# Kernel optimization log

Measured on AMD Instinct MI355X. Metric: run time of the kernel, lower is better.

## Reference

```python
import jax, jax.numpy as jnp
import numpy as np

NTOKENS = 50257
NHID = 1024
NPC = int(np.ceil(np.sqrt(NTOKENS)))            # 225 tokens per class
NCLASSES = int(np.ceil(NTOKENS / NPC))          # 224 classes
BATCH = 1024
INITRANGE = 0.1


def setup_inputs() -> dict:
    key = jax.random.key(0)
    k1, k2, k3, k4 = jax.random.split(key, 4)
    inputs = jax.random.normal(k1, (BATCH, NHID), dtype=jnp.float32)
    labels = jax.random.randint(k2, (BATCH,), 0, NTOKENS, dtype=jnp.int64)
    layer_top_W = jax.random.uniform(k3, (NHID, NCLASSES), minval=-INITRANGE, maxval=INITRANGE, dtype=jnp.float32)
    layer_top_b = jnp.zeros((NCLASSES,), dtype=jnp.float32)
    layer_bottom_W = jax.random.uniform(k4, (NCLASSES, NHID, NPC), minval=-INITRANGE, maxval=INITRANGE, dtype=jnp.float32)
    layer_bottom_b = jnp.zeros((NCLASSES, NPC), dtype=jnp.float32)
    return {
        "inputs": inputs,
        "labels": labels,
        "layer_top_W": layer_top_W,
        "layer_top_b": layer_top_b,
        "layer_bottom_W": layer_bottom_W,
        "layer_bottom_b": layer_bottom_b,
    }


def reference(inputs, labels, layer_top_W, layer_top_b, layer_bottom_W, layer_bottom_b):
    batch_size = inputs.shape[0]
    # decompose label into (class, within-class) position; old-torch `/` on Long == floor div
    pos_top = labels // NPC            # [B]
    pos_bottom = labels % NPC          # [B]

    # top-level class distribution: [B, nclasses]
    top_logits = inputs @ layer_top_W + layer_top_b
    top_probs = jax.nn.softmax(top_logits, axis=1)

    # gather per-sample class weight slices and do batched matvec:
    # layer_bottom_W[pos_top]: [B, nhid, npc]
    bottom_logits = jnp.einsum("bd,bdc->bc", inputs, layer_bottom_W[pos_top]) + layer_bottom_b[pos_top]
    bottom_probs = jax.nn.softmax(bottom_logits, axis=1)

    rows = jnp.arange(batch_size)
    target_probs = top_probs[rows, pos_top] * bottom_probs[rows, pos_bottom]  # [B]
    return target_probs
```

## Files before the change

kernel.cpp:

```cpp
#include <hip/hip_runtime.h>
#include <math.h>

#define NHID 1024
#define NPC  225
#define NCLS 224
#define BATCH 1024
#define NBLK  256

typedef float f4u __attribute__((ext_vector_type(4), aligned(4)));

#define WS_PT 0
#define WS_PB 1024

__global__ __launch_bounds__(1024, 4) void k_fused(const float* __restrict__ X,
                                                   const int* __restrict__ labels,
                                                   const float* __restrict__ Wt,
                                                   const float* __restrict__ bt,
                                                   const float* __restrict__ Wb,
                                                   const float* __restrict__ bb,
                                                   float* __restrict__ ws)
{
    __shared__ __align__(16) float sm[15360];
    __shared__ int cnt_[256];
    __shared__ int iscan_[256];
    __shared__ int slot[8];
    __shared__ int wtot[16];

    const int tid  = threadIdx.x;
    const int wave = tid >> 6;
    const int lane = tid & 63;
    const int j8   = tid & 7;
    const int t8   = tid >> 3;
    const int bid  = blockIdx.x;

    if (tid < 256) cnt_[tid] = 0;
    __syncthreads();
    const int myc = labels[tid] / NPC;
    atomicAdd(&cnt_[myc], 1);
    __syncthreads();
    if (tid < 256) iscan_[tid] = (tid < NCLS) ? ((cnt_[tid] + 7) >> 3) : 0;
    __syncthreads();
    for (int off = 1; off < 256; off <<= 1) {
        int a = 0;
        if (tid < 256 && tid >= off) a = iscan_[tid - off];
        __syncthreads();
        if (tid < 256 && tid >= off) iscan_[tid] += a;
        __syncthreads();
    }
    const int nitems = iscan_[255];

    for (int item = bid; item < nitems; item += NBLK) {
        int lo = 0, hi = NCLS - 1;
        while (lo < hi) {
            const int mid = (lo + hi) >> 1;
            if (iscan_[mid] > item) hi = mid; else lo = mid + 1;
        }
        const int cls    = lo;
        const int ibase  = (cls == 0) ? 0 : iscan_[cls - 1];
        const int within = item - ibase;
        const int nt     = min(8, cnt_[cls] - 8 * within);

        {
            const bool flag = (myc == cls);
            const unsigned long long mb = __ballot(flag);
            if (lane == 0) wtot[wave] = __popcll(mb);
            __syncthreads();
            if (flag) {
                int pos = __popcll(mb & ((1ull << lane) - 1));
#pragma unroll
                for (int w = 0; w < 16; ++w)
                    if (w < wave) pos += wtot[w];
                const int r = pos - 8 * within;
                if (r >= 0 && r < 8) slot[r] = tid;
            }
            __syncthreads();
        }

        const int sid = (j8 < nt) ? slot[j8] : -1;
        for (int d4 = t8; d4 < 256; d4 += 128) {
            float4 v = make_float4(0.f, 0.f, 0.f, 0.f);
            if (sid >= 0) v = ((const float4*)&X[(size_t)sid * NHID])[d4];
            float* p = &sm[48 * d4 + j8];
            p[0] = v.x; p[12] = v.y; p[24] = v.z; p[36] = v.w;
        }
        __syncthreads();

        float acc[8][4];
#pragma unroll
        for (int j = 0; j < 8; ++j)
#pragma unroll
            for (int k = 0; k < 4; ++k) acc[j][k] = 0.f;

        const int d0 = wave * 64;
        const float* Wr = Wb + (size_t)cls * (NHID * NPC) + (size_t)d0 * NPC;

        f4u wbuf[4];
        auto ldrow = [&](int r, f4u& o) {
            const float* p = Wr + (size_t)r * NPC;
            f4u t = {0.f, 0.f, 0.f, 0.f};
            if (lane < 56)       t = __builtin_nontemporal_load((const f4u*)(p + 4 * lane));
            else if (lane == 56) t.x = __builtin_nontemporal_load(p + 224);
            o = t;
        };
        ldrow(0, wbuf[0]); ldrow(1, wbuf[1]); ldrow(2, wbuf[2]); ldrow(3, wbuf[3]);

#pragma unroll 4
        for (int dd = 0; dd < 64; ++dd) {
            const int sl = dd & 3;
            const f4u cw = wbuf[sl];
            ldrow(min(dd + 4, 63), wbuf[sl]);
            const float4 a = *(const float4*)&sm[(d0 + dd) * 12 + 0];
            const float4 b = *(const float4*)&sm[(d0 + dd) * 12 + 4];
            const float xi[8] = {a.x, a.y, a.z, a.w, b.x, b.y, b.z, b.w};
#pragma unroll
            for (int j = 0; j < 8; ++j) {
                acc[j][0] = fmaf(xi[j], cw.x, acc[j][0]);
                acc[j][1] = fmaf(xi[j], cw.y, acc[j][1]);
                acc[j][2] = fmaf(xi[j], cw.z, acc[j][2]);
                acc[j][3] = fmaf(xi[j], cw.w, acc[j][3]);
            }
        }
        __syncthreads();

        float* red = sm;
        if (wave >= 8 && lane <= 56) {
#pragma unroll
            for (int j = 0; j < 8; ++j)
                *(float4*)&red[((wave - 8) * 8 + j) * 240 + 4 * lane] =
                    make_float4(acc[j][0], acc[j][1], acc[j][2], acc[j][3]);
        }
        __syncthreads();
        if (wave < 8 && lane <= 56) {
#pragma unroll
            for (int j = 0; j < 8; ++j) {
                float4* q = (float4*)&red[(wave * 8 + j) * 240 + 4 * lane];
                float4 t = *q;
                t.x += acc[j][0]; t.y += acc[j][1];
                t.z += acc[j][2]; t.w += acc[j][3];
                *q = t;
            }
        }
        __syncthreads();

        if (wave < 8 && wave < nt) {
            const int j = wave;
            const int s = slot[j];
            const int cb = 4 * lane;
            float v0 = -INFINITY, v1 = -INFINITY, v2 = -INFINITY, v3 = -INFINITY;
            if (lane <= 56) {
                float t0 = bb[(size_t)cls * NPC + cb];
                float t1 = (cb + 1 < NPC) ? bb[(size_t)cls * NPC + cb + 1] : 0.f;
                float t2 = (cb + 2 < NPC) ? bb[(size_t)cls * NPC + cb + 2] : 0.f;
                float t3 = (cb + 3 < NPC) ? bb[(size_t)cls * NPC + cb + 3] : 0.f;
#pragma unroll
                for (int g = 0; g < 8; ++g) {
                    const float4 rg = *(const float4*)&red[(g * 8 + j) * 240 + cb];
                    t0 += rg.x; t1 += rg.y; t2 += rg.z; t3 += rg.w;
                }
                v0 = t0;
                v1 = (cb + 1 < NPC) ? t1 : -INFINITY;
                v2 = (cb + 2 < NPC) ? t2 : -INFINITY;
                v3 = (cb + 3 < NPC) ? t3 : -INFINITY;
            }
            float m = fmaxf(fmaxf(v0, v1), fmaxf(v2, v3));
            for (int o = 32; o > 0; o >>= 1) m = fmaxf(m, __shfl_xor(m, o));
            float e = expf(v0 - m) + expf(v1 - m) + expf(v2 - m) + expf(v3 - m);
            for (int o = 32; o > 0; o >>= 1) e += __shfl_xor(e, o);
            const int pb = labels[s] % NPC;
            if (lane == (pb >> 2)) {
                const int kk = pb & 3;
                const float vs = kk == 0 ? v0 : kk == 1 ? v1 : kk == 2 ? v2 : v3;
                ws[WS_PB + s] = expf(vs - m) / e;
            }
        }
        __syncthreads();
    }

    __syncthreads();
    const int sbase = bid * 4;
    {
        const int j4 = tid & 3;
        const int d4 = tid >> 2;
        const float4 xv = ((const float4*)&X[(size_t)(sbase + j4) * NHID])[d4];
        float* p = &sm[16 * d4 + j4];
        p[0] = xv.x; p[4] = xv.y; p[8] = xv.z; p[12] = xv.w;
    }
    __syncthreads();

    float acc[4][4];
#pragma unroll
    for (int j = 0; j < 4; ++j)
#pragma unroll
        for (int k = 0; k < 4; ++k) acc[j][k] = 0.f;

    const int c0 = lane, c1 = lane + 64, c2 = lane + 128, c3 = lane + 192;
    const bool m3 = (c3 < NCLS);
    const int d0 = wave * 64;
    const float* Wr = Wt + (size_t)d0 * NCLS;

    auto ldrowT = [&](int r, float* o) {
        const float* p = Wr + (size_t)r * NCLS;
        o[0] = p[c0]; o[1] = p[c1]; o[2] = p[c2];
        o[3] = m3 ? p[c3] : 0.f;
    };
    float wb[4][4];
    ldrowT(0, wb[0]); ldrowT(1, wb[1]); ldrowT(2, wb[2]); ldrowT(3, wb[3]);

#pragma unroll 4
    for (int dd = 0; dd < 64; ++dd) {
        const int sl = dd & 3;
        const float cw0 = wb[sl][0], cw1 = wb[sl][1],
                    cw2 = wb[sl][2], cw3 = wb[sl][3];
        ldrowT(min(dd + 4, 63), wb[sl]);
        const float4 a = *(const float4*)&sm[4 * (d0 + dd)];
        const float xi[4] = {a.x, a.y, a.z, a.w};
#pragma unroll
        for (int j = 0; j < 4; ++j) {
            acc[j][0] = fmaf(xi[j], cw0, acc[j][0]);
            acc[j][1] = fmaf(xi[j], cw1, acc[j][1]);
            acc[j][2] = fmaf(xi[j], cw2, acc[j][2]);
            acc[j][3] = fmaf(xi[j], cw3, acc[j][3]);
        }
    }
    __syncthreads();

    float* red = sm;
    if (wave >= 8) {
#pragma unroll
        for (int j = 0; j < 4; ++j)
#pragma unroll
            for (int k = 0; k < 4; ++k) {
                const int c = lane + 64 * k;
                if (c < NCLS) red[((wave - 8) * 4 + j) * 232 + c] = acc[j][k];
            }
    }
    __syncthreads();
    if (wave < 8) {
#pragma unroll
        for (int j = 0; j < 4; ++j)
#pragma unroll
            for (int k = 0; k < 4; ++k) {
                const int c = lane + 64 * k;
                if (c < NCLS) red[(wave * 4 + j) * 232 + c] += acc[j][k];
            }
    }
    __syncthreads();

    if (wave < 4) {
        const int j = wave;
        const int s = sbase + j;
        float v0, v1, v2, v3;
        {
            float vv[4];
#pragma unroll
            for (int k = 0; k < 4; ++k) {
                const int c = lane + 64 * k;
                if (c < NCLS) {
                    float t = bt[c];
#pragma unroll
                    for (int g = 0; g < 8; ++g) t += red[(g * 4 + j) * 232 + c];
                    vv[k] = t;
                } else vv[k] = -INFINITY;
            }
            v0 = vv[0]; v1 = vv[1]; v2 = vv[2]; v3 = vv[3];
        }
        float m = fmaxf(fmaxf(v0, v1), fmaxf(v2, v3));
        for (int o = 32; o > 0; o >>= 1) m = fmaxf(m, __shfl_xor(m, o));
        float e = expf(v0 - m) + expf(v1 - m) + expf(v2 - m) + expf(v3 - m);
        for (int o = 32; o > 0; o >>= 1) e += __shfl_xor(e, o);
        const int pt = labels[s] / NPC;
        if (lane == (pt & 63)) {
            const int kk = pt >> 6;
            const float vs = kk == 0 ? v0 : kk == 1 ? v1 : kk == 2 ? v2 : v3;
            ws[WS_PT + s] = expf(vs - m) / e;
        }
    }
}

__global__ void k_mul(const float* __restrict__ ws, float* __restrict__ out)
{
    const int i = blockIdx.x * 256 + threadIdx.x;
    if (i < BATCH) out[i] = ws[WS_PT + i] * ws[WS_PB + i];
}

extern "C" void kernel_launch(void* const* d_in, const int* in_sizes, int n_in,
                              void* d_out, int out_size, void* d_ws, size_t ws_size,
                              hipStream_t stream)
{
    const float* X      = (const float*)d_in[0];
    const int*   labels = (const int*)  d_in[1];
    const float* Wt     = (const float*)d_in[2];
    const float* bt     = (const float*)d_in[3];
    const float* Wb     = (const float*)d_in[4];
    const float* bb     = (const float*)d_in[5];

    hipLaunchKernelGGL(k_fused, dim3(NBLK), dim3(1024), 0, stream,
                       X, labels, Wt, bt, Wb, bb, (float*)d_ws);
    hipLaunchKernelGGL(k_mul, dim3(BATCH / 256), dim3(256), 0, stream,
                       (const float*)d_ws, (float*)d_out);
}
```

Measured before the change: 321.2 us.

## Split top and bottom work into separate blocks with one item per block

The fused kernel now uses 512-thread blocks. The first 128 blocks each compute the top softmax for 8 samples, and up to 352 further blocks each handle one (class, 8-sample) bottom item, replacing the old grid-stride loop in which every block also did a top panel. Both paths share a templated panel8 routine. Each wave now covers 128 hidden rows, so the cross-wave half-reduction step is removed. The intent is to spread work across more independent blocks and shorten the critical path. The risks are that bottom items beyond 352 would be silently dropped, and the bottom weight loads change from float4 to scalar strided loads.

```diff
diff --git a/kernel.cpp b/kernel.cpp
--- a/kernel.cpp
+++ b/kernel.cpp
@@ -5,38 +5,155 @@
 #define NPC  225
 #define NCLS 224
 #define BATCH 1024
-#define NBLK  256
-
-typedef float f4u __attribute__((ext_vector_type(4), aligned(4)));
+#define N_TOPB 128
+#define N_BOTB 352
 
 #define WS_PT 0
 #define WS_PB 1024
 
-__global__ __launch_bounds__(1024, 4) void k_fused(const float* __restrict__ X,
-                                                   const int* __restrict__ labels,
-                                                   const float* __restrict__ Wt,
-                                                   const float* __restrict__ bt,
-                                                   const float* __restrict__ Wb,
-                                                   const float* __restrict__ bb,
-                                                   float* __restrict__ ws)
-{
-    __shared__ __align__(16) float sm[15360];
-    __shared__ int cnt_[256];
-    __shared__ int iscan_[256];
-    __shared__ int slot[8];
-    __shared__ int wtot[16];
-
+template<bool NT>
+__device__ __forceinline__ void panel8(const float* __restrict__ X,
+                                       const int* __restrict__ labels,
+                                       float* sm, const int* slot,
+                                       const float* __restrict__ W, int ncols,
+                                       const float* __restrict__ bias,
+                                       int nt, bool use_mod,
+                                       float* __restrict__ outp)
+{
     const int tid  = threadIdx.x;
     const int wave = tid >> 6;
     const int lane = tid & 63;
     const int j8   = tid & 7;
-    const int t8   = tid >> 3;
+
+    const int sid = (j8 < nt) ? slot[j8] : -1;
+    for (int idx = tid; idx < 2048; idx += 512) {
+        const int d4 = idx >> 3;
+        float4 v = make_float4(0.f, 0.f, 0.f, 0.f);
+        if (sid >= 0) v = ((const float4*)&X[(size_t)sid * NHID])[d4];
+        float* p = &sm[48 * d4 + j8];
+        p[0] = v.x; p[12] = v.y; p[24] = v.z; p[36] = v.w;
+    }
+    __syncthreads();
+
+    float acc[8][4];
+#pragma unroll
+    for (int j = 0; j < 8; ++j)
+#pragma unroll
+        for (int k = 0; k < 4; ++k) acc[j][k] = 0.f;
+
+    const int c0 = lane, c1 = lane + 64, c2 = lane + 128, c3 = lane + 192;
+    const bool m3 = (c3 < ncols);
+    const int d0 = wave * 128;
+    const float* Wr = W + (size_t)d0 * ncols;
+
+    auto ldrow = [&](int r, float* o) {
+        const float* p = Wr + (size_t)r * ncols;
+        if (NT) {
+            o[0] = __builtin_nontemporal_load(p + c0);
+            o[1] = __builtin_nontemporal_load(p + c1);
+            o[2] = __builtin_nontemporal_load(p + c2);
+            o[3] = m3 ? __builtin_nontemporal_load(p + c3) : 0.f;
+        } else {
+            o[0] = p[c0]; o[1] = p[c1]; o[2] = p[c2];
+            o[3] = m3 ? p[c3] : 0.f;
+        }
+    };
+    float wbuf[4][4];
+    ldrow(0, wbuf[0]); ldrow(1, wbuf[1]); ldrow(2, wbuf[2]); ldrow(3, wbuf[3]);
+
+#pragma unroll 4
+    for (int dd = 0; dd < 128; ++dd) {
+        const int sl = dd & 3;
+        const float cw0 = wbuf[sl][0], cw1 = wbuf[sl][1],
+                    cw2 = wbuf[sl][2], cw3 = wbuf[sl][3];
+        ldrow(min(dd + 4, 127), wbuf[sl]);
+        const float4 a = *(const float4*)&sm[(d0 + dd) * 12 + 0];
+        const float4 b = *(const float4*)&sm[(d0 + dd) * 12 + 4];
+        const float xi[8] = {a.x, a.y, a.z, a.w, b.x, b.y, b.z, b.w};
+#pragma unroll
+        for (int j = 0; j < 8; ++j) {
+            acc[j][0] = fmaf(xi[j], cw0, acc[j][0]);
+            acc[j][1] = fmaf(xi[j], cw1, acc[j][1]);
+            acc[j][2] = fmaf(xi[j], cw2, acc[j][2]);
+            acc[j][3] = fmaf(xi[j], cw3, acc[j][3]);
+        }
+    }
+    __syncthreads();
+
+    float* red = sm;
+#pragma unroll
+    for (int j = 0; j < 8; ++j)
+#pragma unroll
+        for (int k = 0; k < 4; ++k) {
+            const int c = lane + 64 * k;
+            if (c < ncols) red[(wave * 8 + j) * 232 + c] = acc[j][k];
+        }
+    __syncthreads();
+
+    if (wave < nt) {
+        const int j = wave;
+        const int s = slot[j];
+        float v0, v1, v2, v3;
+        {
+            float vv[4];
+#pragma unroll
+            for (int k = 0; k < 4; ++k) {
+                const int c = lane + 64 * k;
+                if (c < ncols) {
+                    float t = bias[c];
+#pragma unroll
+                    for (int g = 0; g < 8; ++g) t += red[(g * 8 + j) * 232 + c];
+                    vv[k] = t;
+                } else vv[k] = -INFINITY;
+            }
+            v0 = vv[0]; v1 = vv[1]; v2 = vv[2]; v3 = vv[3];
+        }
+        float m = fmaxf(fmaxf(v0, v1), fmaxf(v2, v3));
+        for (int o = 32; o > 0; o >>= 1) m = fmaxf(m, __shfl_xor(m, o));
+        float e = expf(v0 - m) + expf(v1 - m) + expf(v2 - m) + expf(v3 - m);
+        for (int o = 32; o > 0; o >>= 1) e += __shfl_xor(e, o);
+        const int lab  = labels[s];
+        const int pick = use_mod ? (lab % NPC) : (lab / NPC);
+        if (lane == (pick & 63)) {
+            const int kk = pick >> 6;
+            const float vs = kk == 0 ? v0 : kk == 1 ? v1 : kk == 2 ? v2 : v3;
+            outp[s] = expf(vs - m) / e;
+        }
+    }
+}
+
+__global__ __launch_bounds__(512, 4) void k_fused(const float* __restrict__ X,
+                                                  const int* __restrict__ labels,
+                                                  const float* __restrict__ Wt,
+                                                  const float* __restrict__ bt,
+                                                  const float* __restrict__ Wb,
+                                                  const float* __restrict__ bb,
+                                                  float* __restrict__ ws)
+{
+    __shared__ __align__(16) float sm[14848];
+    __shared__ int cnt_[256];
+    __shared__ int iscan_[256];
+    __shared__ int slot[8];
+    __shared__ int wtA[8], wtB[8];
+
+    const int tid  = threadIdx.x;
+    const int wave = tid >> 6;
+    const int lane = tid & 63;
     const int bid  = blockIdx.x;
 
+    if (bid < N_TOPB) {
+        if (tid < 8) slot[tid] = bid * 8 + tid;
+        __syncthreads();
+        panel8<false>(X, labels, sm, slot, Wt, NCLS, bt, 8, false, ws + WS_PT);
+        return;
+    }
+
     if (tid < 256) cnt_[tid] = 0;
     __syncthreads();
-    const int myc = labels[tid] / NPC;
-    atomicAdd(&cnt_[myc], 1);
+    const int la = labels[tid] / NPC;
+    const int lb = labels[tid + 512] / NPC;
+    atomicAdd(&cnt_[la], 1);
+    atomicAdd(&cnt_[lb], 1);
     __syncthreads();
     if (tid < 256) iscan_[tid] = (tid < NCLS) ? ((cnt_[tid] + 7) >> 3) : 0;
     __syncthreads();
@@ -47,234 +164,44 @@
         if (tid < 256 && tid >= off) iscan_[tid] += a;
         __syncthreads();
     }
-    const int nitems = iscan_[255];
-
-    for (int item = bid; item < nitems; item += NBLK) {
-        int lo = 0, hi = NCLS - 1;
-        while (lo < hi) {
-            const int mid = (lo + hi) >> 1;
-            if (iscan_[mid] > item) hi = mid; else lo = mid + 1;
-        }
-        const int cls    = lo;
-        const int ibase  = (cls == 0) ? 0 : iscan_[cls - 1];
-        const int within = item - ibase;
-        const int nt     = min(8, cnt_[cls] - 8 * within);
-
-        {
-            const bool flag = (myc == cls);
-            const unsigned long long mb = __ballot(flag);
-            if (lane == 0) wtot[wave] = __popcll(mb);
-            __syncthreads();
-            if (flag) {
-                int pos = __popcll(mb & ((1ull << lane) - 1));
-#pragma unroll
-                for (int w = 0; w < 16; ++w)
-                    if (w < wave) pos += wtot[w];
-                const int r = pos - 8 * within;
-                if (r >= 0 && r < 8) slot[r] = tid;
-            }
-            __syncthreads();
-        }
-
-        const int sid = (j8 < nt) ? slot[j8] : -1;
-        for (int d4 = t8; d4 < 256; d4 += 128) {
-            float4 v = make_float4(0.f, 0.f, 0.f, 0.f);
-            if (sid >= 0) v = ((const float4*)&X[(size_t)sid * NHID])[d4];
-            float* p = &sm[48 * d4 + j8];
-            p[0] = v.x; p[12] = v.y; p[24] = v.z; p[36] = v.w;
-        }
-        __syncthreads();
-
-        float acc[8][4];
-#pragma unroll
-        for (int j = 0; j < 8; ++j)
-#pragma unroll
-            for (int k = 0; k < 4; ++k) acc[j][k] = 0.f;
-
-        const int d0 = wave * 64;
-        const float* Wr = Wb + (size_t)cls * (NHID * NPC) + (size_t)d0 * NPC;
-
-        f4u wbuf[4];
-        auto ldrow = [&](int r, f4u& o) {
-            const float* p = Wr + (size_t)r * NPC;
-            f4u t = {0.f, 0.f, 0.f, 0.f};
-            if (lane < 56)       t = __builtin_nontemporal_load((const f4u*)(p + 4 * lane));
-            else if (lane == 56) t.x = __builtin_nontemporal_load(p + 224);
-            o = t;
-        };
-        ldrow(0, wbuf[0]); ldrow(1, wbuf[1]); ldrow(2, wbuf[2]); ldrow(3, wbuf[3]);
-
-#pragma unroll 4
-        for (int dd = 0; dd < 64; ++dd) {
-            const int sl = dd & 3;
-            const f4u cw = wbuf[sl];
-            ldrow(min(dd + 4, 63), wbuf[sl]);
-            const float4 a = *(const float4*)&sm[(d0 + dd) * 12 + 0];
-            const float4 b = *(const float4*)&sm[(d0 + dd) * 12 + 4];
-            const float xi[8] = {a.x, a.y, a.z, a.w, b.x, b.y, b.z, b.w};
-#pragma unroll
-            for (int j = 0; j < 8; ++j) {
-                acc[j][0] = fmaf(xi[j], cw.x, acc[j][0]);
-                acc[j][1] = fmaf(xi[j], cw.y, acc[j][1]);
-                acc[j][2] = fmaf(xi[j], cw.z, acc[j][2]);
-                acc[j][3] = fmaf(xi[j], cw.w, acc[j][3]);
-            }
-        }
-        __syncthreads();
-
-        float* red = sm;
-        if (wave >= 8 && lane <= 56) {
-#pragma unroll
-            for (int j = 0; j < 8; ++j)
-                *(float4*)&red[((wave - 8) * 8 + j) * 240 + 4 * lane] =
-                    make_float4(acc[j][0], acc[j][1], acc[j][2], acc[j][3]);
-        }
-        __syncthreads();
-        if (wave < 8 && lane <= 56) {
-#pragma unroll
-            for (int j = 0; j < 8; ++j) {
-                float4* q = (float4*)&red[(wave * 8 + j) * 240 + 4 * lane];
-                float4 t = *q;
-                t.x += acc[j][0]; t.y += acc[j][1];
-                t.z += acc[j][2]; t.w += acc[j][3];
-                *q = t;
-            }
-        }
-        __syncthreads();
-
-        if (wave < 8 && wave < nt) {
-            const int j = wave;
-            const int s = slot[j];
-            const int cb = 4 * lane;
-            float v0 = -INFINITY, v1 = -INFINITY, v2 = -INFINITY, v3 = -INFINITY;
-            if (lane <= 56) {
-                float t0 = bb[(size_t)cls * NPC + cb];
-                float t1 = (cb + 1 < NPC) ? bb[(size_t)cls * NPC + cb + 1] : 0.f;
-                float t2 = (cb + 2 < NPC) ? bb[(size_t)cls * NPC + cb + 2] : 0.f;
-                float t3 = (cb + 3 < NPC) ? bb[(size_t)cls * NPC + cb + 3] : 0.f;
-#pragma unroll
-                for (int g = 0; g < 8; ++g) {
-                    const float4 rg = *(const float4*)&red[(g * 8 + j) * 240 + cb];
-                    t0 += rg.x; t1 += rg.y; t2 += rg.z; t3 += rg.w;
-                }
-                v0 = t0;
-                v1 = (cb + 1 < NPC) ? t1 : -INFINITY;
-                v2 = (cb + 2 < NPC) ? t2 : -INFINITY;
-                v3 = (cb + 3 < NPC) ? t3 : -INFINITY;
-            }
-            float m = fmaxf(fmaxf(v0, v1), fmaxf(v2, v3));
-            for (int o = 32; o > 0; o >>= 1) m = fmaxf(m, __shfl_xor(m, o));
-            float e = expf(v0 - m) + expf(v1 - m) + expf(v2 - m) + expf(v3 - m);
-            for (int o = 32; o > 0; o >>= 1) e += __shfl_xor(e, o);
-            const int pb = labels[s] % NPC;
-            if (lane == (pb >> 2)) {
-                const int kk = pb & 3;
-                const float vs = kk == 0 ? v0 : kk == 1 ? v1 : kk == 2 ? v2 : v3;
-                ws[WS_PB + s] = expf(vs - m) / e;
-            }
-        }
-        __syncthreads();
-    }
-
-    __syncthreads();
-    const int sbase = bid * 4;
-    {
-        const int j4 = tid & 3;
-        const int d4 = tid >> 2;
-        const float4 xv = ((const float4*)&X[(size_t)(sbase + j4) * NHID])[d4];
-        float* p = &sm[16 * d4 + j4];
-        p[0] = xv.x; p[4] = xv.y; p[8] = xv.z; p[12] = xv.w;
-    }
-    __syncthreads();
-
-    float acc[4][4];
-#pragma unroll
-    for (int j = 0; j < 4; ++j)
-#pragma unroll
-        for (int k = 0; k < 4; ++k) acc[j][k] = 0.f;
-
-    const int c0 = lane, c1 = lane + 64, c2 = lane + 128, c3 = lane + 192;
-    const bool m3 = (c3 < NCLS);
-    const int d0 = wave * 64;
-    const float* Wr = Wt + (size_t)d0 * NCLS;
-
-    auto ldrowT = [&](int r, float* o) {
-        const float* p = Wr + (size_t)r * NCLS;
-        o[0] = p[c0]; o[1] = p[c1]; o[2] = p[c2];
-        o[3] = m3 ? p[c3] : 0.f;
-    };
-    float wb[4][4];
-    ldrowT(0, wb[0]); ldrowT(1, wb[1]); ldrowT(2, wb[2]); ldrowT(3, wb[3]);
-
-#pragma unroll 4
-    for (int dd = 0; dd < 64; ++dd) {
-        const int sl = dd & 3;
-        const float cw0 = wb[sl][0], cw1 = wb[sl][1],
-                    cw2 = wb[sl][2], cw3 = wb[sl][3];
-        ldrowT(min(dd + 4, 63), wb[sl]);
-        const float4 a = *(const float4*)&sm[4 * (d0 + dd)];
-        const float xi[4] = {a.x, a.y, a.z, a.w};
-#pragma unroll
-        for (int j = 0; j < 4; ++j) {
-            acc[j][0] = fmaf(xi[j], cw0, acc[j][0]);
-            acc[j][1] = fmaf(xi[j], cw1, acc[j][1]);
-            acc[j][2] = fmaf(xi[j], cw2, acc[j][2]);
-            acc[j][3] = fmaf(xi[j], cw3, acc[j][3]);
-        }
-    }
-    __syncthreads();
-
-    float* red = sm;
-    if (wave >= 8) {
-#pragma unroll
-        for (int j = 0; j < 4; ++j)
-#pragma unroll
-            for (int k = 0; k < 4; ++k) {
-                const int c = lane + 64 * k;
-                if (c < NCLS) red[((wave - 8) * 4 + j) * 232 + c] = acc[j][k];
-            }
-    }
-    __syncthreads();
-    if (wave < 8) {
-#pragma unroll
-        for (int j = 0; j < 4; ++j)
-#pragma unroll
-            for (int k = 0; k < 4; ++k) {
-                const int c = lane + 64 * k;
-                if (c < NCLS) red[(wave * 4 + j) * 232 + c] += acc[j][k];
-            }
-    }
-    __syncthreads();
-
-    if (wave < 4) {
-        const int j = wave;
-        const int s = sbase + j;
-        float v0, v1, v2, v3;
-        {
-            float vv[4];
-#pragma unroll
-            for (int k = 0; k < 4; ++k) {
-                const int c = lane + 64 * k;
-                if (c < NCLS) {
-                    float t = bt[c];
-#pragma unroll
-                    for (int g = 0; g < 8; ++g) t += red[(g * 4 + j) * 232 + c];
-                    vv[k] = t;
-                } else vv[k] = -INFINITY;
-            }
-            v0 = vv[0]; v1 = vv[1]; v2 = vv[2]; v3 = vv[3];
-        }
-        float m = fmaxf(fmaxf(v0, v1), fmaxf(v2, v3));
-        for (int o = 32; o > 0; o >>= 1) m = fmaxf(m, __shfl_xor(m, o));
-        float e = expf(v0 - m) + expf(v1 - m) + expf(v2 - m) + expf(v3 - m);
-        for (int o = 32; o > 0; o >>= 1) e += __shfl_xor(e, o);
-        const int pt = labels[s] / NPC;
-        if (lane == (pt & 63)) {
-            const int kk = pt >> 6;
-            const float vs = kk == 0 ? v0 : kk == 1 ? v1 : kk == 2 ? v2 : v3;
-            ws[WS_PT + s] = expf(vs - m) / e;
-        }
-    }
+    const int item = bid - N_TOPB;
+    if (item >= iscan_[255]) return;
+
+    int lo = 0, hi = NCLS - 1;
+    while (lo < hi) {
+        const int mid = (lo + hi) >> 1;
+        if (iscan_[mid] > item) hi = mid; else lo = mid + 1;
+    }
+    const int cls    = lo;
+    const int ibase  = (cls == 0) ? 0 : iscan_[cls - 1];
+    const int within = item - ibase;
+    const int nt     = min(8, cnt_[cls] - 8 * within);
+
+    const bool fA = (la == cls), fB = (lb == cls);
+    const unsigned long long mA = __ballot(fA);
+    const unsigned long long mB = __ballot(fB);
+    if (lane == 0) { wtA[wave] = __popcll(mA); wtB[wave] = __popcll(mB); }
+    __syncthreads();
+    int preA = 0, preB = 0, totA = 0;
+#pragma unroll
+    for (int w = 0; w < 8; ++w) {
+        totA += wtA[w];
+        if (w < wave) { preA += wtA[w]; preB += wtB[w]; }
+    }
+    preB += totA;
+    if (fA) {
+        const int r = preA + (int)__popcll(mA & ((1ull << lane) - 1)) - 8 * within;
+        if (r >= 0 && r < 8) slot[r] = tid;
+    }
+    if (fB) {
+        const int r = preB + (int)__popcll(mB & ((1ull << lane) - 1)) - 8 * within;
+        if (r >= 0 && r < 8) slot[r] = tid + 512;
+    }
+    __syncthreads();
+
+    panel8<true>(X, labels, sm, slot,
+                 Wb + (size_t)cls * (NHID * NPC), NPC,
+                 bb + (size_t)cls * NPC, nt, true, ws + WS_PB);
 }
 
 __global__ void k_mul(const float* __restrict__ ws, float* __restrict__ out)
@@ -294,7 +221,7 @@
     const float* Wb     = (const float*)d_in[4];
     const float* bb     = (const float*)d_in[5];
 
-    hipLaunchKernelGGL(k_fused, dim3(NBLK), dim3(1024), 0, stream,
+    hipLaunchKernelGGL(k_fused, dim3(N_TOPB + N_BOTB), dim3(512), 0, stream,
                        X, labels, Wt, bt, Wb, bb, (float*)d_ws);
     hipLaunchKernelGGL(k_mul, dim3(BATCH / 256), dim3(256), 0, stream,
                        (const float*)d_ws, (float*)d_out);
```

Result: faster. 295.8 us (-7.9%).
